# Kernel optimization log

Hardware: AMD Instinct MI355X
Metric: run time of the kernel (lower is better)

The kernel has to match this reference:

```python
import jax, jax.numpy as jnp
import numpy as np
from jax import lax

B, C, H, W = 2, 192, 256, 256
HEADS = 4
EPS = 1e-12  # F.normalize clamp_min eps


def conv1x1(w, x):
    # w: [O, I, 1, 1], x: [B, I, H, W] -> [B, O, H, W]
    return jnp.einsum('oi,bihw->bohw', w[:, :, 0, 0], x)


def setup_inputs() -> dict:
    key = jax.random.key(0)
    ks = jax.random.split(key, 8)
    s = 0.05
    return {
        'x': jax.random.normal(ks[0], (B, C, H, W), dtype=jnp.float32),
        'noise_map': jax.random.uniform(ks[1], (B, 1, 1, 1), dtype=jnp.float32),
        'base_temp': jnp.ones((HEADS, 1, 1), dtype=jnp.float32),
        'w_nm1': jax.random.normal(ks[2], (C // 4, 1, 1, 1), dtype=jnp.float32) * s,
        'w_nm2': jax.random.normal(ks[3], (HEADS, C // 4, 1, 1), dtype=jnp.float32) * s,
        'w_qkv': jax.random.normal(ks[4], (3 * C, C, 1, 1), dtype=jnp.float32) * s,
        'w_dw': jax.random.normal(ks[5], (3 * C, 1, 3, 3), dtype=jnp.float32) * s,
        'w_out': jax.random.normal(ks[6], (C, C, 1, 1), dtype=jnp.float32) * s,
    }


def reference(x, noise_map, base_temp, w_nm1, w_nm2, w_qkv, w_dw, w_out):
    b, c, h, w = x.shape
    ch = c // HEADS  # channels per head

    # qkv 1x1 conv followed by depthwise 3x3 conv
    qkv = conv1x1(w_qkv, x)
    qkv = lax.conv_general_dilated(
        qkv, w_dw, window_strides=(1, 1), padding='SAME',
        feature_group_count=3 * c,
        dimension_numbers=('NCHW', 'OIHW', 'NCHW'))
    q, k, v = jnp.split(qkv, 3, axis=1)

    def heads(t):  # [b, c, h, w] -> [b, head, ch, h*w]
        return t.reshape(b, HEADS, ch, h * w)

    q, k, v = heads(q), heads(k), heads(v)

    # L2 normalize over spatial dim (matches F.normalize eps clamp)
    q = q / jnp.maximum(jnp.linalg.norm(q, axis=-1, keepdims=True), EPS)
    k = k / jnp.maximum(jnp.linalg.norm(k, axis=-1, keepdims=True), EPS)

    # noise modulation MLP (1x1 convs on [b,1,1,1] noise map)
    nm = conv1x1(w_nm1, noise_map)
    nm = jnp.where(nm >= 0, nm, 0.2 * nm)  # LeakyReLU(0.2)
    nm = jax.nn.sigmoid(conv1x1(w_nm2, nm))  # [b, heads, 1, 1]
    noise_weight = nm.reshape(b, HEADS, 1, 1)
    temp = base_temp[None] * (2.0 - noise_weight)  # [b, heads, 1, 1]

    # channel (transposed) attention: [b, head, ch, ch]
    attn = jnp.einsum('bhcn,bhdn->bhcd', q, k) * temp
    attn = jax.nn.softmax(attn, axis=-1)
    out = jnp.einsum('bhcd,bhdn->bhcn', attn, v)

    out = out.reshape(b, c, h, w)
    return conv1x1(w_out, out)
```

## Files before the change

### kernel.cpp

```cpp
#include <hip/hip_runtime.h>
#include <hip/hip_bf16.h>

#define NPIX 65536
#define IW 256

typedef unsigned short ushort_t;
typedef __attribute__((ext_vector_type(8))) short bf16x8;
typedef __attribute__((ext_vector_type(4))) float f32x4;

__device__ __forceinline__ float b2f(ushort_t u) {
    union { unsigned int i; float f; } v;
    v.i = ((unsigned int)u) << 16;
    return v.f;
}
__device__ __forceinline__ ushort_t f2b(float f) {
    __hip_bfloat16 h = __float2bfloat16(f);
    return *reinterpret_cast<ushort_t*>(&h);
}

template<int B_F32, int A_BF16, int OUT_BF16>
__global__ __launch_bounds__(256) void kgemm_fused(const void* __restrict__ Aptr,
                                                   const void* __restrict__ Bsrc,
                                                   void* __restrict__ Cout,
                                                   int mtiles, long Astr, long Bstr, long Cstr) {
    __shared__ ushort_t Bs[128 * 200];
    __shared__ ushort_t AsLu[64 * 200];
    const int tid = threadIdx.x;
    const int lane = tid & 63;
    const int wave = tid >> 6;
    const int batch = blockIdx.y;
    const long n_base = (long)blockIdx.x * 128;

    ushort_t (*Lu)[66] = reinterpret_cast<ushort_t (*)[66]>(AsLu);
    #pragma unroll
    for (int half = 0; half < 2; half++) {
        const long n0 = n_base + half * 64;
        __syncthreads();
        #pragma unroll
        for (int i = 0; i < 24; i++) {
            int e = tid + i * 256;
            int k = e >> 5, n2 = e & 31;
            ushort2 o;
            if (B_F32) {
                float2 v = *reinterpret_cast<const float2*>(
                    (const float*)Bsrc + batch * Bstr + (long)k * NPIX + n0 + n2 * 2);
                o = make_ushort2(f2b(v.x), f2b(v.y));
            } else {
                o = *reinterpret_cast<const ushort2*>(
                    (const ushort_t*)Bsrc + batch * Bstr + (long)k * NPIX + n0 + n2 * 2);
            }
            *reinterpret_cast<ushort2*>(&Lu[k][n2 * 2]) = o;
        }
        __syncthreads();
        const int n = tid >> 2, seg = tid & 3;
        const int kb = seg * 48;
        ushort_t* dst = &Bs[(half * 64 + n) * 200 + kb];
        #pragma unroll
        for (int w = 0; w < 6; w++) {
            unsigned int p0 = (unsigned int)Lu[kb + w * 8 + 0][n] | ((unsigned int)Lu[kb + w * 8 + 1][n] << 16);
            unsigned int p1 = (unsigned int)Lu[kb + w * 8 + 2][n] | ((unsigned int)Lu[kb + w * 8 + 3][n] << 16);
            unsigned int p2 = (unsigned int)Lu[kb + w * 8 + 4][n] | ((unsigned int)Lu[kb + w * 8 + 5][n] << 16);
            unsigned int p3 = (unsigned int)Lu[kb + w * 8 + 6][n] | ((unsigned int)Lu[kb + w * 8 + 7][n] << 16);
            *reinterpret_cast<int4*>(dst + w * 8) = make_int4(p0, p1, p2, p3);
        }
    }

    const int r15 = lane & 15;
    const int g8 = (lane >> 4) * 8;
    const int gq = (lane >> 4) * 4;
    const int nw = wave * 32;

    for (int mt = 0; mt < mtiles; mt++) {
        const int m_base = mt * 64;
        __syncthreads();
        #pragma unroll
        for (int i = 0; i < 12; i++) {
            int c = tid + i * 256;
            int m = c / 48, k4 = c % 48;
            if (A_BF16) {
                const ushort_t* A = (const ushort_t*)Aptr + batch * Astr;
                ushort4 v = *reinterpret_cast<const ushort4*>(A + (long)(m_base + m) * 192 + k4 * 4);
                *reinterpret_cast<ushort4*>(&AsLu[m * 200 + k4 * 4]) = v;
            } else {
                const float* A = (const float*)Aptr + batch * Astr;
                float4 v = *reinterpret_cast<const float4*>(A + (long)(m_base + m) * 192 + k4 * 4);
                ushort4 o = make_ushort4(f2b(v.x), f2b(v.y), f2b(v.z), f2b(v.w));
                *reinterpret_cast<ushort4*>(&AsLu[m * 200 + k4 * 4]) = o;
            }
        }
        __syncthreads();

        f32x4 acc[4][2];
        #pragma unroll
        for (int mi = 0; mi < 4; mi++)
            #pragma unroll
            for (int ni = 0; ni < 2; ni++)
                acc[mi][ni] = (f32x4){0.f, 0.f, 0.f, 0.f};

        #pragma unroll
        for (int kk = 0; kk < 192; kk += 32) {
            bf16x8 a[4], b[2];
            #pragma unroll
            for (int mi = 0; mi < 4; mi++)
                a[mi] = *reinterpret_cast<const bf16x8*>(&AsLu[(mi * 16 + r15) * 200 + kk + g8]);
            #pragma unroll
            for (int ni = 0; ni < 2; ni++)
                b[ni] = *reinterpret_cast<const bf16x8*>(&Bs[(nw + ni * 16 + r15) * 200 + kk + g8]);
            #pragma unroll
            for (int mi = 0; mi < 4; mi++)
                #pragma unroll
                for (int ni = 0; ni < 2; ni++)
                    acc[mi][ni] = __builtin_amdgcn_mfma_f32_16x16x32_bf16(a[mi], b[ni], acc[mi][ni], 0, 0, 0);
        }

        #pragma unroll
        for (int mi = 0; mi < 4; mi++)
            #pragma unroll
            for (int ni = 0; ni < 2; ni++)
                #pragma unroll
                for (int r = 0; r < 4; r++) {
                    long m = m_base + mi * 16 + gq + r;
                    long n = n_base + nw + ni * 16 + r15;
                    if (OUT_BF16) ((ushort_t*)Cout)[batch * Cstr + m * NPIX + n] = f2b(acc[mi][ni][r]);
                    else          ((float*)Cout)[batch * Cstr + m * NPIX + n] = acc[mi][ni][r];
                }
    }
}

__global__ __launch_bounds__(256) void kdw_conv(const ushort_t* __restrict__ qkvb,
                                                const float* __restrict__ wdw,
                                                ushort_t* __restrict__ dwb,
                                                ushort_t* __restrict__ dwv,
                                                long qstr, long dbstr, long dvstr) {
    __shared__ ushort_t rows[18][IW];
    const int tid = threadIdx.x;
    const int j = blockIdx.y;
    const int batch = blockIdx.z;
    const int y0 = blockIdx.x * 16;
    const ushort_t* src = qkvb + batch * qstr + (long)j * NPIX;
    ushort_t* dst = (j < 384) ? (dwb + batch * dbstr + (long)j * NPIX)
                              : (dwv + batch * dvstr + (long)(j - 384) * NPIX);
    float wv[9];
    #pragma unroll
    for (int t = 0; t < 9; t++) wv[t] = wdw[j * 9 + t];

    for (int e = tid; e < 18 * 64; e += 256) {
        int r = e >> 6, x4 = e & 63;
        int yy = y0 - 1 + r;
        ushort4 val = (yy >= 0 && yy <= 255)
            ? *reinterpret_cast<const ushort4*>(src + yy * IW + x4 * 4)
            : make_ushort4(0, 0, 0, 0);
        *reinterpret_cast<ushort4*>(&rows[r][x4 * 4]) = val;
    }
    __syncthreads();

    const int ty = tid >> 4;
    const int tx = (tid & 15) * 16;
    float win[3][18];
    #pragma unroll
    for (int dy = 0; dy < 3; dy++) {
        const ushort_t* rw = rows[ty + dy];
        win[dy][0] = (tx > 0) ? b2f(rw[tx - 1]) : 0.f;
        #pragma unroll
        for (int i = 0; i < 16; i++) win[dy][i + 1] = b2f(rw[tx + i]);
        win[dy][17] = (tx < 240) ? b2f(rw[tx + 16]) : 0.f;
    }

    unsigned int packed[8];
    #pragma unroll
    for (int p2 = 0; p2 < 8; p2++) {
        unsigned int pk = 0;
        #pragma unroll
        for (int half = 0; half < 2; half++) {
            const int p = p2 * 2 + half;
            float a = 0.f;
            #pragma unroll
            for (int dy = 0; dy < 3; dy++)
                #pragma unroll
                for (int dx = 0; dx < 3; dx++)
                    a += wv[dy * 3 + dx] * win[dy][p + dx];
            pk |= ((unsigned int)f2b(a)) << (16 * half);
        }
        packed[p2] = pk;
    }
    int4* dp = reinterpret_cast<int4*>(dst + (y0 + ty) * IW + tx);
    dp[0] = make_int4(packed[0], packed[1], packed[2], packed[3]);
    dp[1] = make_int4(packed[4], packed[5], packed[6], packed[7]);
}

__global__ __launch_bounds__(256) void k2_gram_mfma(const ushort_t* __restrict__ dwb,
                                                    float* __restrict__ Spt,
                                                    float* __restrict__ sqp,
                                                    long dbstr, long Sptstr, long sqpstr) {
    const int tid = threadIdx.x;
    const int lane = tid & 63;
    const int wave = tid >> 6;
    const int chunk = blockIdx.x;
    const int h = blockIdx.y;
    const int batch = blockIdx.z;
    const int r15 = lane & 15;
    const int g = lane >> 4;
    const long n0 = (long)chunk * 1024 + wave * 256;
    const ushort_t* qb = dwb + batch * dbstr + (long)(h * 48) * NPIX + n0;
    const ushort_t* kb = dwb + batch * dbstr + (long)(192 + h * 48) * NPIX + n0;

    f32x4 acc[3][3];
    #pragma unroll
    for (int mi = 0; mi < 3; mi++)
        #pragma unroll
        for (int nj = 0; nj < 3; nj++)
            acc[mi][nj] = (f32x4){0.f, 0.f, 0.f, 0.f};
    float ssq[3] = {0.f, 0.f, 0.f}, ssk[3] = {0.f, 0.f, 0.f};

    for (int ks = 0; ks < 8; ks++) {
        const int off = ks * 32 + g * 8;
        bf16x8 a[3], bfr[3];
        #pragma unroll
        for (int mi = 0; mi < 3; mi++)
            a[mi] = *reinterpret_cast<const bf16x8*>(qb + (long)(mi * 16 + r15) * NPIX + off);
        #pragma unroll
        for (int nj = 0; nj < 3; nj++)
            bfr[nj] = *reinterpret_cast<const bf16x8*>(kb + (long)(nj * 16 + r15) * NPIX + off);
        #pragma unroll
        for (int mi = 0; mi < 3; mi++)
            #pragma unroll
            for (int j = 0; j < 8; j++) {
                float f = b2f((ushort_t)a[mi][j]);
                ssq[mi] += f * f;
            }
        #pragma unroll
        for (int nj = 0; nj < 3; nj++)
            #pragma unroll
            for (int j = 0; j < 8; j++) {
                float f = b2f((ushort_t)bfr[nj][j]);
                ssk[nj] += f * f;
            }
        #pragma unroll
        for (int mi = 0; mi < 3; mi++)
            #pragma unroll
            for (int nj = 0; nj < 3; nj++)
                acc[mi][nj] = __builtin_amdgcn_mfma_f32_16x16x32_bf16(a[mi], bfr[nj], acc[mi][nj], 0, 0, 0);
    }

    const int cw = chunk * 4 + wave;
    float* outb = Spt + batch * Sptstr + (long)cw * 9216 + h * 2304;
    const int gq = g * 4;
    #pragma unroll
    for (int mi = 0; mi < 3; mi++)
        #pragma unroll
        for (int nj = 0; nj < 3; nj++)
            #pragma unroll
            for (int r = 0; r < 4; r++)
                outb[(mi * 16 + gq + r) * 48 + nj * 16 + r15] = acc[mi][nj][r];

    #pragma unroll
    for (int mi = 0; mi < 3; mi++) {
        ssq[mi] += __shfl_xor(ssq[mi], 16, 64);
        ssq[mi] += __shfl_xor(ssq[mi], 32, 64);
        ssk[mi] += __shfl_xor(ssk[mi], 16, 64);
        ssk[mi] += __shfl_xor(ssk[mi], 32, 64);
    }
    if (lane < 16) {
        float* sqb = sqp + batch * sqpstr + (long)cw * 384;
        #pragma unroll
        for (int mi = 0; mi < 3; mi++) {
            sqb[h * 48 + mi * 16 + lane] = ssq[mi];
            sqb[192 + h * 48 + mi * 16 + lane] = ssk[mi];
        }
    }
}

__global__ __launch_bounds__(256) void k3a_reduce2(const float* __restrict__ Spt,
                                                   const float* __restrict__ sqp,
                                                   float* __restrict__ S1,
                                                   float* __restrict__ sq1,
                                                   long Sptstr, long sqpstr, long S1str, long sq1str) {
    const int seg = blockIdx.y;
    const int batch = blockIdx.z;
    const int w = blockIdx.x * 256 + threadIdx.x;
    if (w < 9216) {
        const float* p = Spt + batch * Sptstr + (long)seg * 32 * 9216 + w;
        float s = 0.f;
        for (int i = 0; i < 32; i++) s += p[(long)i * 9216];
        S1[batch * S1str + seg * 9216 + w] = s;
    } else if (w < 9600) {
        const int c = w - 9216;
        const float* p = sqp + batch * sqpstr + (long)seg * 32 * 384 + c;
        float s = 0.f;
        for (int i = 0; i < 32; i++) s += p[i * 384];
        sq1[batch * sq1str + seg * 384 + c] = s;
    }
}

__global__ __launch_bounds__(256) void k3b_attn_weff(const float* __restrict__ S1,
                                                     const float* __restrict__ sq1,
                                                     const float* __restrict__ noise,
                                                     const float* __restrict__ btemp,
                                                     const float* __restrict__ w_nm1,
                                                     const float* __restrict__ w_nm2,
                                                     const float* __restrict__ w_out,
                                                     ushort_t* __restrict__ weffb,
                                                     int b0, long S1str, long sq1str, long wstr) {
    __shared__ float sA[48][49];
    __shared__ float invq[48], invk[48];
    __shared__ float stemp;
    const int h = blockIdx.x, batch = blockIdx.y, tid = threadIdx.x;
    const float* S1b = S1 + batch * S1str;
    const float* sq1b = sq1 + batch * sq1str;
    for (int e = tid; e < 2304; e += 256) {
        float s = 0.f;
        #pragma unroll
        for (int seg = 0; seg < 8; seg++) s += S1b[seg * 9216 + h * 2304 + e];
        sA[e / 48][e % 48] = s;
    }
    if (tid < 96) {
        int c = (tid < 48) ? (h * 48 + tid) : (192 + h * 48 + (tid - 48));
        float s = 0.f;
        #pragma unroll
        for (int seg = 0; seg < 8; seg++) s += sq1b[seg * 384 + c];
        float inv = 1.f / fmaxf(sqrtf(s), 1e-12f);
        if (tid < 48) invq[tid] = inv; else invk[tid - 48] = inv;
    }
    if (tid == 0) {
        float nz = noise[b0 + batch];
        float a = 0.f;
        for (int i = 0; i < 48; i++) {
            float t = w_nm1[i] * nz;
            t = (t >= 0.f) ? t : 0.2f * t;
            a += w_nm2[h * 48 + i] * t;
        }
        float sig = 1.f / (1.f + expf(-a));
        stemp = btemp[h] * (2.f - sig);
    }
    __syncthreads();
    for (int e = tid; e < 2304; e += 256) {
        int c = e / 48, d = e % 48;
        sA[c][d] *= invq[c] * invk[d] * stemp;
    }
    __syncthreads();
    if (tid < 48) {
        float m = -1e30f;
        for (int d = 0; d < 48; d++) m = fmaxf(m, sA[tid][d]);
        float sum = 0.f;
        for (int d = 0; d < 48; d++) {
            float e_ = expf(sA[tid][d] - m);
            sA[tid][d] = e_;
            sum += e_;
        }
        float r = 1.f / sum;
        for (int d = 0; d < 48; d++) sA[tid][d] *= r;
    }
    __syncthreads();
    ushort_t* wb = weffb + batch * wstr;
    for (int e = tid; e < 9216; e += 256) {
        int o = e / 48, d = e % 48;
        const float* wr = w_out + o * 192 + h * 48;
        float s = 0.f;
        #pragma unroll
        for (int c = 0; c < 48; c++) s += wr[c] * sA[c][d];
        wb[o * 192 + h * 48 + d] = f2b(s);
    }
}

extern "C" void kernel_launch(void* const* d_in, const int* in_sizes, int n_in,
                              void* d_out, int out_size, void* d_ws, size_t ws_size,
                              hipStream_t stream) {
    const float* x      = (const float*)d_in[0];
    const float* noise  = (const float*)d_in[1];
    const float* btemp  = (const float*)d_in[2];
    const float* w_nm1  = (const float*)d_in[3];
    const float* w_nm2  = (const float*)d_in[4];
    const float* w_qkv  = (const float*)d_in[5];
    const float* w_dw   = (const float*)d_in[6];
    const float* w_out  = (const float*)d_in[7];
    float* out = (float*)d_out;
    float* ws = (float*)d_ws;

    const long need2 = 80603136L;
    if ((long)(ws_size / 4) >= need2) {
        ushort_t* qkvb = (ushort_t*)ws;
        ushort_t* dwv  = (ushort_t*)(ws + 37748736);
        ushort_t* dwb  = (ushort_t*)(ws + 50331648);
        float* Spt  = ws + 75497472;
        float* sqp  = ws + 80216064;
        float* S1   = ws + 80412672;
        float* sq1  = ws + 80560128;
        ushort_t* weffb = (ushort_t*)(ws + 80566272);

        kgemm_fused<1, 0, 1><<<dim3(512, 2), 256, 0, stream>>>(
            w_qkv, x, qkvb, 9, 0L, 192L * NPIX, 576L * NPIX);
        kdw_conv<<<dim3(16, 576, 2), 256, 0, stream>>>(
            qkvb, w_dw, dwb, dwv, 576L * NPIX, 384L * NPIX, 192L * NPIX);
        k2_gram_mfma<<<dim3(64, 4, 2), 256, 0, stream>>>(
            dwb, Spt, sqp, 384L * NPIX, 2359296L, 98304L);
        k3a_reduce2<<<dim3(38, 8, 2), 256, 0, stream>>>(
            Spt, sqp, S1, sq1, 2359296L, 98304L, 73728L, 3072L);
        k3b_attn_weff<<<dim3(4, 2), 256, 0, stream>>>(
            S1, sq1, noise, btemp, w_nm1, w_nm2, w_out, weffb, 0, 73728L, 3072L, 36864L);
        kgemm_fused<0, 1, 0><<<dim3(512, 2), 256, 0, stream>>>(
            weffb, dwv, out, 3, 36864L, 192L * NPIX, 192L * NPIX);
    } else {
        ushort_t* qkvb = (ushort_t*)ws;
        float* Spt  = ws;
        float* sqp  = ws + 9437184;
        float* S1   = ws + 9830400;
        float* sq1  = ws + 9904128;
        ushort_t* weffb = (ushort_t*)(ws + 9907200);
        ushort_t* dwv = (ushort_t*)(ws + 18874368);
        ushort_t* dwb = (ushort_t*)(ws + 25427968);

        for (int b = 0; b < 2; b++) {
            const float* xb = x + (long)b * 192 * NPIX;
            float* outb = out + (long)b * 192 * NPIX;
            kgemm_fused<1, 0, 1><<<dim3(512, 1), 256, 0, stream>>>(
                w_qkv, xb, qkvb, 9, 0L, 0L, 0L);
            kdw_conv<<<dim3(16, 576, 1), 256, 0, stream>>>(
                qkvb, w_dw, dwb, dwv, 0L, 0L, 0L);
            k2_gram_mfma<<<dim3(64, 4, 1), 256, 0, stream>>>(
                dwb, Spt, sqp, 0L, 0L, 0L);
            k3a_reduce2<<<dim3(38, 8, 1), 256, 0, stream>>>(
                Spt, sqp, S1, sq1, 0L, 0L, 0L, 0L);
            k3b_attn_weff<<<dim3(4, 1), 256, 0, stream>>>(
                S1, sq1, noise, btemp, w_nm1, w_nm2, w_out, weffb, b, 0L, 0L, 0L);
            kgemm_fused<0, 1, 0><<<dim3(512, 1), 256, 0, stream>>>(
                weffb, dwv, outb, 3, 0L, 0L, 0L);
        }
    }
}
```

Baseline: 250.1 us.

## Halve GEMM N-tile and prefetch next A tile into registers

The fused 1x1-conv GEMM kernel now handles 64 pixels per block instead of 128, so it launches twice as many blocks and uses less shared memory per block. Each wave computes one 16-column slice. The next 64-row tile of A is loaded from global memory into registers while the current tile is being computed, which hides that load latency. The trade-off is that A weights are re-read by twice as many blocks, and each wave does fewer MFMAs per LDS load of A.

```diff
diff --git a/kernel.cpp b/kernel.cpp
--- a/kernel.cpp
+++ b/kernel.cpp
@@ -23,38 +23,50 @@
                                                    const void* __restrict__ Bsrc,
                                                    void* __restrict__ Cout,
                                                    int mtiles, long Astr, long Bstr, long Cstr) {
-    __shared__ ushort_t Bs[128 * 200];
+    __shared__ ushort_t Bs[64 * 200];
     __shared__ ushort_t AsLu[64 * 200];
     const int tid = threadIdx.x;
     const int lane = tid & 63;
     const int wave = tid >> 6;
     const int batch = blockIdx.y;
-    const long n_base = (long)blockIdx.x * 128;
+    const long n_base = (long)blockIdx.x * 64;
+
+    ushort4 areg[12];
+    #pragma unroll
+    for (int i = 0; i < 12; i++) {
+        int c = tid + i * 256;
+        int m = c / 48, k4 = c % 48;
+        if (A_BF16) {
+            const ushort_t* A = (const ushort_t*)Aptr + batch * Astr;
+            areg[i] = *reinterpret_cast<const ushort4*>(A + (long)m * 192 + k4 * 4);
+        } else {
+            const float* A = (const float*)Aptr + batch * Astr;
+            float4 v = *reinterpret_cast<const float4*>(A + (long)m * 192 + k4 * 4);
+            areg[i] = make_ushort4(f2b(v.x), f2b(v.y), f2b(v.z), f2b(v.w));
+        }
+    }
 
     ushort_t (*Lu)[66] = reinterpret_cast<ushort_t (*)[66]>(AsLu);
     #pragma unroll
-    for (int half = 0; half < 2; half++) {
-        const long n0 = n_base + half * 64;
-        __syncthreads();
-        #pragma unroll
-        for (int i = 0; i < 24; i++) {
-            int e = tid + i * 256;
-            int k = e >> 5, n2 = e & 31;
-            ushort2 o;
-            if (B_F32) {
-                float2 v = *reinterpret_cast<const float2*>(
-                    (const float*)Bsrc + batch * Bstr + (long)k * NPIX + n0 + n2 * 2);
-                o = make_ushort2(f2b(v.x), f2b(v.y));
-            } else {
-                o = *reinterpret_cast<const ushort2*>(
-                    (const ushort_t*)Bsrc + batch * Bstr + (long)k * NPIX + n0 + n2 * 2);
-            }
-            *reinterpret_cast<ushort2*>(&Lu[k][n2 * 2]) = o;
-        }
-        __syncthreads();
+    for (int i = 0; i < 24; i++) {
+        int e = tid + i * 256;
+        int k = e >> 5, n2 = e & 31;
+        ushort2 o;
+        if (B_F32) {
+            float2 v = *reinterpret_cast<const float2*>(
+                (const float*)Bsrc + batch * Bstr + (long)k * NPIX + n_base + n2 * 2);
+            o = make_ushort2(f2b(v.x), f2b(v.y));
+        } else {
+            o = *reinterpret_cast<const ushort2*>(
+                (const ushort_t*)Bsrc + batch * Bstr + (long)k * NPIX + n_base + n2 * 2);
+        }
+        *reinterpret_cast<ushort2*>(&Lu[k][n2 * 2]) = o;
+    }
+    __syncthreads();
+    {
         const int n = tid >> 2, seg = tid & 3;
         const int kb = seg * 48;
-        ushort_t* dst = &Bs[(half * 64 + n) * 200 + kb];
+        ushort_t* dst = &Bs[n * 200 + kb];
         #pragma unroll
         for (int w = 0; w < 6; w++) {
             unsigned int p0 = (unsigned int)Lu[kb + w * 8 + 0][n] | ((unsigned int)Lu[kb + w * 8 + 1][n] << 16);
@@ -63,67 +75,66 @@
             unsigned int p3 = (unsigned int)Lu[kb + w * 8 + 6][n] | ((unsigned int)Lu[kb + w * 8 + 7][n] << 16);
             *reinterpret_cast<int4*>(dst + w * 8) = make_int4(p0, p1, p2, p3);
         }
+        if (seg == 3)
+            *reinterpret_cast<int4*>(&Bs[n * 200 + 192]) = make_int4(0, 0, 0, 0);
     }
 
     const int r15 = lane & 15;
     const int g8 = (lane >> 4) * 8;
     const int gq = (lane >> 4) * 4;
-    const int nw = wave * 32;
+    const int nw = wave * 16;
 
     for (int mt = 0; mt < mtiles; mt++) {
-        const int m_base = mt * 64;
         __syncthreads();
         #pragma unroll
         for (int i = 0; i < 12; i++) {
             int c = tid + i * 256;
             int m = c / 48, k4 = c % 48;
-            if (A_BF16) {
-                const ushort_t* A = (const ushort_t*)Aptr + batch * Astr;
-                ushort4 v = *reinterpret_cast<const ushort4*>(A + (long)(m_base + m) * 192 + k4 * 4);
-                *reinterpret_cast<ushort4*>(&AsLu[m * 200 + k4 * 4]) = v;
-            } else {
-                const float* A = (const float*)Aptr + batch * Astr;
-                float4 v = *reinterpret_cast<const float4*>(A + (long)(m_base + m) * 192 + k4 * 4);
-                ushort4 o = make_ushort4(f2b(v.x), f2b(v.y), f2b(v.z), f2b(v.w));
-                *reinterpret_cast<ushort4*>(&AsLu[m * 200 + k4 * 4]) = o;
+            *reinterpret_cast<ushort4*>(&AsLu[m * 200 + k4 * 4]) = areg[i];
+        }
+        if (mt + 1 < mtiles) {
+            #pragma unroll
+            for (int i = 0; i < 12; i++) {
+                int c = tid + i * 256;
+                int m = (mt + 1) * 64 + c / 48, k4 = c % 48;
+                if (A_BF16) {
+                    const ushort_t* A = (const ushort_t*)Aptr + batch * Astr;
+                    areg[i] = *reinterpret_cast<const ushort4*>(A + (long)m * 192 + k4 * 4);
+                } else {
+                    const float* A = (const float*)Aptr + batch * Astr;
+                    float4 v = *reinterpret_cast<const float4*>(A + (long)m * 192 + k4 * 4);
+                    areg[i] = make_ushort4(f2b(v.x), f2b(v.y), f2b(v.z), f2b(v.w));
+                }
             }
         }
         __syncthreads();
 
-        f32x4 acc[4][2];
-        #pragma unroll
-        for (int mi = 0; mi < 4; mi++)
-            #pragma unroll
-            for (int ni = 0; ni < 2; ni++)
-                acc[mi][ni] = (f32x4){0.f, 0.f, 0.f, 0.f};
+        f32x4 acc[4];
+        #pragma unroll
+        for (int mi = 0; mi < 4; mi++) acc[mi] = (f32x4){0.f, 0.f, 0.f, 0.f};
 
         #pragma unroll
         for (int kk = 0; kk < 192; kk += 32) {
-            bf16x8 a[4], b[2];
+            bf16x8 b = *reinterpret_cast<const bf16x8*>(&Bs[(nw + r15) * 200 + kk + g8]);
+            bf16x8 a[4];
             #pragma unroll
             for (int mi = 0; mi < 4; mi++)
                 a[mi] = *reinterpret_cast<const bf16x8*>(&AsLu[(mi * 16 + r15) * 200 + kk + g8]);
             #pragma unroll
-            for (int ni = 0; ni < 2; ni++)
-                b[ni] = *reinterpret_cast<const bf16x8*>(&Bs[(nw + ni * 16 + r15) * 200 + kk + g8]);
-            #pragma unroll
             for (int mi = 0; mi < 4; mi++)
-                #pragma unroll
-                for (int ni = 0; ni < 2; ni++)
-                    acc[mi][ni] = __builtin_amdgcn_mfma_f32_16x16x32_bf16(a[mi], b[ni], acc[mi][ni], 0, 0, 0);
-        }
-
+                acc[mi] = __builtin_amdgcn_mfma_f32_16x16x32_bf16(a[mi], b, acc[mi], 0, 0, 0);
+        }
+
+        const int m_base = mt * 64;
         #pragma unroll
         for (int mi = 0; mi < 4; mi++)
             #pragma unroll
-            for (int ni = 0; ni < 2; ni++)
-                #pragma unroll
-                for (int r = 0; r < 4; r++) {
-                    long m = m_base + mi * 16 + gq + r;
-                    long n = n_base + nw + ni * 16 + r15;
-                    if (OUT_BF16) ((ushort_t*)Cout)[batch * Cstr + m * NPIX + n] = f2b(acc[mi][ni][r]);
-                    else          ((float*)Cout)[batch * Cstr + m * NPIX + n] = acc[mi][ni][r];
-                }
+            for (int r = 0; r < 4; r++) {
+                long m = m_base + mi * 16 + gq + r;
+                long n = n_base + nw + r15;
+                if (OUT_BF16) ((ushort_t*)Cout)[batch * Cstr + m * NPIX + n] = f2b(acc[mi][r]);
+                else          ((float*)Cout)[batch * Cstr + m * NPIX + n] = acc[mi][r];
+            }
     }
 }
 
@@ -387,7 +398,7 @@
         float* sq1  = ws + 80560128;
         ushort_t* weffb = (ushort_t*)(ws + 80566272);
 
-        kgemm_fused<1, 0, 1><<<dim3(512, 2), 256, 0, stream>>>(
+        kgemm_fused<1, 0, 1><<<dim3(1024, 2), 256, 0, stream>>>(
             w_qkv, x, qkvb, 9, 0L, 192L * NPIX, 576L * NPIX);
         kdw_conv<<<dim3(16, 576, 2), 256, 0, stream>>>(
             qkvb, w_dw, dwb, dwv, 576L * NPIX, 384L * NPIX, 192L * NPIX);
@@ -397,7 +408,7 @@
             Spt, sqp, S1, sq1, 2359296L, 98304L, 73728L, 3072L);
         k3b_attn_weff<<<dim3(4, 2), 256, 0, stream>>>(
             S1, sq1, noise, btemp, w_nm1, w_nm2, w_out, weffb, 0, 73728L, 3072L, 36864L);
-        kgemm_fused<0, 1, 0><<<dim3(512, 2), 256, 0, stream>>>(
+        kgemm_fused<0, 1, 0><<<dim3(1024, 2), 256, 0, stream>>>(
             weffb, dwv, out, 3, 36864L, 192L * NPIX, 192L * NPIX);
     } else {
         ushort_t* qkvb = (ushort_t*)ws;
@@ -412,7 +423,7 @@
         for (int b = 0; b < 2; b++) {
             const float* xb = x + (long)b * 192 * NPIX;
             float* outb = out + (long)b * 192 * NPIX;
-            kgemm_fused<1, 0, 1><<<dim3(512, 1), 256, 0, stream>>>(
+            kgemm_fused<1, 0, 1><<<dim3(1024, 1), 256, 0, stream>>>(
                 w_qkv, xb, qkvb, 9, 0L, 0L, 0L);
             kdw_conv<<<dim3(16, 576, 1), 256, 0, stream>>>(
                 qkvb, w_dw, dwb, dwv, 0L, 0L, 0L);
@@ -422,7 +433,7 @@
                 Spt, sqp, S1, sq1, 0L, 0L, 0L, 0L);
             k3b_attn_weff<<<dim3(4, 1), 256, 0, stream>>>(
                 S1, sq1, noise, btemp, w_nm1, w_nm2, w_out, weffb, b, 0L, 0L, 0L);
-            kgemm_fused<0, 1, 0><<<dim3(512, 1), 256, 0, stream>>>(
+            kgemm_fused<0, 1, 0><<<dim3(1024, 1), 256, 0, stream>>>(
                 weffb, dwv, outb, 3, 0L, 0L, 0L);
         }
     }
```

After: 291.2 us. 16.4% more time.
